# Kernel tuning notes

Measured on AMD Instinct MI355X. Metric: run time of the kernel, lower is better.

The kernel has to match this reference:

```python
import jax, jax.numpy as jnp
import numpy as np

B, N, F_IN, F_OUT = 8, 2048, 256, 128
ALPHA = 0.2  # LeakyReLU negative slope
NEG_BIG = -9e15


def setup_inputs() -> dict:
    key = jax.random.key(0)
    k1, k2, k3, k4 = jax.random.split(key, 4)
    h = jax.random.normal(k1, (B, N, F_IN), dtype=jnp.float32)
    adj = jax.random.randint(k2, (B, N, N), 0, 2, dtype=jnp.int32)
    W = jax.random.normal(k3, (F_IN, F_OUT), dtype=jnp.float32) * 0.05
    a = jax.random.normal(k4, (2 * F_OUT,), dtype=jnp.float32) * 0.05
    return {"h": h, "adj": adj, "W": W, "a": a}


def reference(h, adj, W, a):
    # Wh: [B, N, F_OUT]
    Wh = jnp.einsum("bnf,fo->bno", h, W)
    # a([Wh_i || Wh_j]) decomposes: e_ij = a1.Wh_i + a2.Wh_j  (avoids [B,N*N,2F] tensor)
    a1, a2 = a[:F_OUT], a[F_OUT:]
    s1 = jnp.einsum("bno,o->bn", Wh, a1)  # [B, N]
    s2 = jnp.einsum("bno,o->bn", Wh, a2)  # [B, N]
    e = jax.nn.leaky_relu(s1[:, :, None] + s2[:, None, :], negative_slope=ALPHA)  # [B,N,N]
    e = jnp.where(adj > 0, e, NEG_BIG)
    attention = jax.nn.softmax(e, axis=2)
    # dropout is identity (eval / p=0)
    h_prime = jnp.einsum("bij,bjo->bio", attention, Wh)  # [B, N, F_OUT]
    return h_prime
```

## Files before the change

kernel.cpp:

```cpp
#include <hip/hip_runtime.h>

#define NB 8
#define NN 2048
#define FIN 256
#define FOUT 128

typedef __attribute__((ext_vector_type(8))) short short8;
typedef __attribute__((ext_vector_type(4))) float f32x4;

static __device__ __forceinline__ unsigned short f2bf(float f) {
    unsigned int u = __float_as_uint(f);
    u += 0x7fffu + ((u >> 16) & 1u);
    return (unsigned short)(u >> 16);
}

__global__ __launch_bounds__(256) void gat_prep(
    const float* __restrict__ h, const float* __restrict__ W, const float* __restrict__ a,
    unsigned short* __restrict__ whpv, float* __restrict__ s1g, float* __restrict__ s2g)
{
    __shared__ __align__(16) float hT[64 * FIN];
    __shared__ __align__(16) unsigned short pvs[8192];
    const int t = threadIdx.x;
    const int bx = blockIdx.x;
    const int b = bx >> 5;
    const int jt = bx & 31;
    const int j0 = jt * 64;

    const float* hsrc = h + ((size_t)b * NN + j0) * FIN;
    #pragma unroll
    for (int p = 0; p < 16; ++p) {
        int idx = p * 256 + t;
        *(f32x4*)&hT[idx * 4] = *(const f32x4*)&hsrc[idx * 4];
    }
    __syncthreads();

    const int cg = t & 31;
    const int rg = t >> 5;
    float acc[8][4];
    #pragma unroll
    for (int r = 0; r < 8; ++r)
        #pragma unroll
        for (int q = 0; q < 4; ++q) acc[r][q] = 0.f;

    for (int f = 0; f < FIN; f += 4) {
        f32x4 wv[4];
        #pragma unroll
        for (int q = 0; q < 4; ++q) wv[q] = *(const f32x4*)&W[(f + q) * FOUT + cg * 4];
        #pragma unroll
        for (int r = 0; r < 8; ++r) {
            f32x4 hv = *(const f32x4*)&hT[(rg * 8 + r) * FIN + f];
            #pragma unroll
            for (int q = 0; q < 4; ++q) {
                acc[r][0] += hv[q] * wv[q][0];
                acc[r][1] += hv[q] * wv[q][1];
                acc[r][2] += hv[q] * wv[q][2];
                acc[r][3] += hv[q] * wv[q][3];
            }
        }
    }

    f32x4 a1v = *(const f32x4*)&a[cg * 4];
    f32x4 a2v = *(const f32x4*)&a[FOUT + cg * 4];
    #pragma unroll
    for (int r = 0; r < 8; ++r) {
        float p1 = acc[r][0]*a1v[0] + acc[r][1]*a1v[1] + acc[r][2]*a1v[2] + acc[r][3]*a1v[3];
        float p2 = acc[r][0]*a2v[0] + acc[r][1]*a2v[1] + acc[r][2]*a2v[2] + acc[r][3]*a2v[3];
        #pragma unroll
        for (int m = 16; m >= 1; m >>= 1) {
            p1 += __shfl_xor(p1, m, 64);
            p2 += __shfl_xor(p2, m, 64);
        }
        if (cg == 0) {
            s1g[b * NN + j0 + rg * 8 + r] = p1;
            s2g[b * NN + j0 + rg * 8 + r] = p2;
        }
    }

    #pragma unroll
    for (int r = 0; r < 8; ++r) {
        int jl = rg * 8 + r;
        int kt = jl >> 5, j5 = jl & 31, g = j5 >> 3, i = j5 & 7;
        #pragma unroll
        for (int q = 0; q < 4; ++q) {
            int c = cg * 4 + q;
            int lane = g * 16 + (c & 15);
            int nt = c >> 4;
            pvs[((kt * 8 + nt) * 64 + lane) * 8 + i] = f2bf(acc[r][q]);
        }
    }
    __syncthreads();
    unsigned short* dst = whpv + (size_t)(b * 32 + jt) * 8192;
    #pragma unroll
    for (int p = 0; p < 4; ++p) {
        int idx = p * 2048 + t * 8;
        *(short8*)&dst[idx] = *(const short8*)&pvs[idx];
    }
}

__global__ __launch_bounds__(512, 4) void gat_main(
    const int* __restrict__ adj, const unsigned short* __restrict__ whpv,
    const float* __restrict__ s1g, const float* __restrict__ s2g, float* __restrict__ out)
{
    __shared__ __align__(16) char Plds[2][32 * 128];
    __shared__ __align__(16) unsigned short BL[2][8192];
    __shared__ float Sden[32];

    const int t = threadIdx.x;
    const int bx = blockIdx.x;
    const int b = bx >> 6;
    const int i0 = (bx & 63) * 32;

    const int r  = t >> 4;
    const int jq = t & 15;

    const int lane = t & 63;
    const int w = t >> 6;
    const int mt = w & 1;
    const int nb = w >> 1;
    const int arow = mt * 16 + (lane & 15);
    const int g = lane >> 4;

    const float s1v = s1g[b * NN + i0 + r];

    f32x4 acc[2];
    acc[0] = (f32x4){0.f, 0.f, 0.f, 0.f};
    acc[1] = (f32x4){0.f, 0.f, 0.f, 0.f};
    float ssum = 0.f;

    const int* adjb = adj + (size_t)b * NN * NN + (size_t)i0 * NN;
    const int* aptr = adjb + (size_t)r * NN + jq * 4;
    const unsigned short* whb = whpv + (size_t)b * 32 * 8192;
    const float* s2b = s2g + b * NN;

    int4 ac = *(const int4*)aptr;
    short8 wc0 = *(const short8*)&whb[t * 8];
    short8 wc1 = *(const short8*)&whb[4096 + t * 8];

    const int pbyte = r * 128 + ((jq >> 1) ^ (r & 7)) * 16 + (jq & 1) * 8;
    const int abyte = arow * 128;
    int buf = 0;

    for (int jc = 0; jc < 32; ++jc) {
        const int jn = (jc + 1) & 31;
        int4 an = *(const int4*)(aptr + jn * 64);
        const unsigned short* wn = whb + (size_t)jn * 8192;
        short8 wn0 = *(const short8*)&wn[t * 8];
        short8 wn1 = *(const short8*)&wn[4096 + t * 8];

        f32x4 s2v = *(const f32x4*)&s2b[jc * 64 + jq * 4];
        float p[4];
        {
            float e0 = s1v + s2v[0]; e0 = fmaxf(e0, 0.2f * e0);
            p[0] = (ac.x > 0) ? __expf(e0) : 0.f;
            float e1 = s1v + s2v[1]; e1 = fmaxf(e1, 0.2f * e1);
            p[1] = (ac.y > 0) ? __expf(e1) : 0.f;
            float e2 = s1v + s2v[2]; e2 = fmaxf(e2, 0.2f * e2);
            p[2] = (ac.z > 0) ? __expf(e2) : 0.f;
            float e3 = s1v + s2v[3]; e3 = fmaxf(e3, 0.2f * e3);
            p[3] = (ac.w > 0) ? __expf(e3) : 0.f;
        }
        ssum += (p[0] + p[1]) + (p[2] + p[3]);
        unsigned int pk0 = (unsigned int)f2bf(p[0]) | ((unsigned int)f2bf(p[1]) << 16);
        unsigned int pk1 = (unsigned int)f2bf(p[2]) | ((unsigned int)f2bf(p[3]) << 16);
        uint2 pk = {pk0, pk1};
        *(uint2*)&Plds[buf][pbyte] = pk;

        *(short8*)&BL[buf][t * 8] = wc0;
        *(short8*)&BL[buf][4096 + t * 8] = wc1;
        __syncthreads();

        #pragma unroll
        for (int kt = 0; kt < 2; ++kt) {
            int aslot = (4 * kt + g) ^ (arow & 7);
            short8 af = *(const short8*)&Plds[buf][abyte + aslot * 16];
            #pragma unroll
            for (int n = 0; n < 2; ++n) {
                int nt = nb * 2 + n;
                short8 bfr = *(const short8*)&BL[buf][((kt * 8 + nt) * 64 + lane) * 8];
                acc[n] = __builtin_amdgcn_mfma_f32_16x16x32_bf16(af, bfr, acc[n], 0, 0, 0);
            }
        }

        ac = an; wc0 = wn0; wc1 = wn1; buf ^= 1;
    }

    {
        float v = ssum;
        #pragma unroll
        for (int m = 8; m >= 1; m >>= 1) v += __shfl_xor(v, m, 64);
        if (jq == 0) Sden[r] = v;
    }
    __syncthreads();

    float* ob = out + ((size_t)b * NN + i0) * FOUT;
    #pragma unroll
    for (int n = 0; n < 2; ++n) {
        int col = (nb * 2 + n) * 16 + (lane & 15);
        #pragma unroll
        for (int q = 0; q < 4; ++q) {
            int row = mt * 16 + (lane >> 4) * 4 + q;
            ob[(size_t)row * FOUT + col] = acc[n][q] / Sden[row];
        }
    }
}

extern "C" void kernel_launch(void* const* d_in, const int* in_sizes, int n_in,
                              void* d_out, int out_size, void* d_ws, size_t ws_size,
                              hipStream_t stream) {
    (void)in_sizes; (void)n_in; (void)out_size; (void)ws_size;
    const float* h   = (const float*)d_in[0];
    const int*   adj = (const int*)d_in[1];
    const float* W   = (const float*)d_in[2];
    const float* a   = (const float*)d_in[3];
    float* out = (float*)d_out;

    unsigned short* whpv = (unsigned short*)d_ws;
    float* s1g = (float*)((char*)d_ws + (4u << 20));
    float* s2g = (float*)((char*)d_ws + (4u << 20) + (64u << 10));

    gat_prep<<<dim3(256), dim3(256), 0, stream>>>(h, W, a, whpv, s1g, s2g);
    gat_main<<<dim3(512), dim3(512), 0, stream>>>(adj, whpv, s1g, s2g, out);
}
```

Baseline: 79.47 us.

## Batch four j-chunks per barrier with deeper prefetch and swizzled block order

```diff
diff --git a/kernel.cpp b/kernel.cpp
--- a/kernel.cpp
+++ b/kernel.cpp
@@ -13,6 +13,20 @@
     u += 0x7fffu + ((u >> 16) & 1u);
     return (unsigned short)(u >> 16);
 }
+
+static __device__ __forceinline__ unsigned int cvtpk(float lo, float hi) {
+    unsigned int d;
+    asm("v_cvt_pk_bf16_f32 %0, %1, %2" : "=v"(d) : "v"(lo), "v"(hi));
+    return d;
+}
+
+#define BAR_LGKM()                                            \
+    do {                                                      \
+        asm volatile("s_waitcnt lgkmcnt(0)" ::: "memory");    \
+        __builtin_amdgcn_sched_barrier(0);                    \
+        __builtin_amdgcn_s_barrier();                         \
+        __builtin_amdgcn_sched_barrier(0);                    \
+    } while (0)
 
 __global__ __launch_bounds__(256) void gat_prep(
     const float* __restrict__ h, const float* __restrict__ W, const float* __restrict__ a,
@@ -101,14 +115,14 @@
     const int* __restrict__ adj, const unsigned short* __restrict__ whpv,
     const float* __restrict__ s1g, const float* __restrict__ s2g, float* __restrict__ out)
 {
-    __shared__ __align__(16) char Plds[2][32 * 128];
-    __shared__ __align__(16) unsigned short BL[2][8192];
-    __shared__ float Sden[32];
+    __shared__ __align__(16) char pool[81920];
+    unsigned short* BL = (unsigned short*)pool;
+    char* Plds = pool + 65536;
 
     const int t = threadIdx.x;
     const int bx = blockIdx.x;
-    const int b = bx >> 6;
-    const int i0 = (bx & 63) * 32;
+    const int b  = bx & 7;
+    const int i0 = (bx >> 3) * 32;
 
     const int r  = t >> 4;
     const int jq = t & 15;
@@ -127,63 +141,78 @@
     acc[1] = (f32x4){0.f, 0.f, 0.f, 0.f};
     float ssum = 0.f;
 
-    const int* adjb = adj + (size_t)b * NN * NN + (size_t)i0 * NN;
-    const int* aptr = adjb + (size_t)r * NN + jq * 4;
+    const int* aptr = adj + (size_t)b * NN * NN + (size_t)(i0 + r) * NN + jq * 4;
     const unsigned short* whb = whpv + (size_t)b * 32 * 8192;
     const float* s2b = s2g + b * NN;
 
-    int4 ac = *(const int4*)aptr;
-    short8 wc0 = *(const short8*)&whb[t * 8];
-    short8 wc1 = *(const short8*)&whb[4096 + t * 8];
+    int4   ac0, ac1, ac2, ac3;
+    short8 wa0, wa1, wa2, wa3, wb0, wb1, wb2, wb3;
+    f32x4  s20, s21, s22, s23;
+
+#define PRELOAD(C)                                                          \
+    ac##C = *(const int4*)(aptr + (C) * 64);                                \
+    wa##C = *(const short8*)&whb[(size_t)(C) * 8192 + t * 8];               \
+    wb##C = *(const short8*)&whb[(size_t)(C) * 8192 + 4096 + t * 8];        \
+    s2##C = *(const f32x4*)&s2b[(C) * 64 + jq * 4];
+
+    PRELOAD(0) PRELOAD(1) PRELOAD(2) PRELOAD(3)
+#undef PRELOAD
 
     const int pbyte = r * 128 + ((jq >> 1) ^ (r & 7)) * 16 + (jq & 1) * 8;
     const int abyte = arow * 128;
-    int buf = 0;
-
-    for (int jc = 0; jc < 32; ++jc) {
-        const int jn = (jc + 1) & 31;
-        int4 an = *(const int4*)(aptr + jn * 64);
-        const unsigned short* wn = whb + (size_t)jn * 8192;
-        short8 wn0 = *(const short8*)&wn[t * 8];
-        short8 wn1 = *(const short8*)&wn[4096 + t * 8];
-
-        f32x4 s2v = *(const f32x4*)&s2b[jc * 64 + jq * 4];
-        float p[4];
-        {
-            float e0 = s1v + s2v[0]; e0 = fmaxf(e0, 0.2f * e0);
-            p[0] = (ac.x > 0) ? __expf(e0) : 0.f;
-            float e1 = s1v + s2v[1]; e1 = fmaxf(e1, 0.2f * e1);
-            p[1] = (ac.y > 0) ? __expf(e1) : 0.f;
-            float e2 = s1v + s2v[2]; e2 = fmaxf(e2, 0.2f * e2);
-            p[2] = (ac.z > 0) ? __expf(e2) : 0.f;
-            float e3 = s1v + s2v[3]; e3 = fmaxf(e3, 0.2f * e3);
-            p[3] = (ac.w > 0) ? __expf(e3) : 0.f;
-        }
-        ssum += (p[0] + p[1]) + (p[2] + p[3]);
-        unsigned int pk0 = (unsigned int)f2bf(p[0]) | ((unsigned int)f2bf(p[1]) << 16);
-        unsigned int pk1 = (unsigned int)f2bf(p[2]) | ((unsigned int)f2bf(p[3]) << 16);
-        uint2 pk = {pk0, pk1};
-        *(uint2*)&Plds[buf][pbyte] = pk;
-
-        *(short8*)&BL[buf][t * 8] = wc0;
-        *(short8*)&BL[buf][4096 + t * 8] = wc1;
-        __syncthreads();
-
-        #pragma unroll
-        for (int kt = 0; kt < 2; ++kt) {
-            int aslot = (4 * kt + g) ^ (arow & 7);
-            short8 af = *(const short8*)&Plds[buf][abyte + aslot * 16];
-            #pragma unroll
-            for (int n = 0; n < 2; ++n) {
-                int nt = nb * 2 + n;
-                short8 bfr = *(const short8*)&BL[buf][((kt * 8 + nt) * 64 + lane) * 8];
-                acc[n] = __builtin_amdgcn_mfma_f32_16x16x32_bf16(af, bfr, acc[n], 0, 0, 0);
-            }
-        }
-
-        ac = an; wc0 = wn0; wc1 = wn1; buf ^= 1;
-    }
-
+
+#define PPHASE(C, S)                                                        \
+    do {                                                                    \
+        int4   a_  = ac##C;                                                 \
+        short8 w0_ = wa##C;                                                 \
+        short8 w1_ = wb##C;                                                 \
+        f32x4  s2v = s2##C;                                                 \
+        const int jn = ((S) * 4 + 4 + (C)) & 31;                            \
+        ac##C = *(const int4*)(aptr + jn * 64);                             \
+        wa##C = *(const short8*)&whb[(size_t)jn * 8192 + t * 8];            \
+        wb##C = *(const short8*)&whb[(size_t)jn * 8192 + 4096 + t * 8];     \
+        s2##C = *(const f32x4*)&s2b[jn * 64 + jq * 4];                      \
+        float e0 = s1v + s2v[0]; e0 = fmaxf(e0, 0.2f * e0);                 \
+        float p0 = (a_.x > 0) ? __expf(e0) : 0.f;                           \
+        float e1 = s1v + s2v[1]; e1 = fmaxf(e1, 0.2f * e1);                 \
+        float p1 = (a_.y > 0) ? __expf(e1) : 0.f;                           \
+        float e2 = s1v + s2v[2]; e2 = fmaxf(e2, 0.2f * e2);                 \
+        float p2 = (a_.z > 0) ? __expf(e2) : 0.f;                           \
+        float e3 = s1v + s2v[3]; e3 = fmaxf(e3, 0.2f * e3);                 \
+        float p3 = (a_.w > 0) ? __expf(e3) : 0.f;                           \
+        ssum += (p0 + p1) + (p2 + p3);                                      \
+        uint2 pk = {cvtpk(p0, p1), cvtpk(p2, p3)};                          \
+        *(uint2*)&Plds[(C) * 4096 + pbyte] = pk;                            \
+        *(short8*)&BL[(C) * 8192 + t * 8] = w0_;                            \
+        *(short8*)&BL[(C) * 8192 + 4096 + t * 8] = w1_;                     \
+    } while (0)
+
+#define MPHASE(C)                                                           \
+    do {                                                                    \
+        _Pragma("unroll")                                                   \
+        for (int kt = 0; kt < 2; ++kt) {                                    \
+            const int aslot = (4 * kt + g) ^ (arow & 7);                    \
+            short8 af = *(const short8*)&Plds[(C) * 4096 + abyte + aslot * 16]; \
+            _Pragma("unroll")                                               \
+            for (int n = 0; n < 2; ++n) {                                   \
+                const int nt = nb * 2 + n;                                  \
+                short8 bfr = *(const short8*)&BL[(C) * 8192 + ((kt * 8 + nt) * 64 + lane) * 8]; \
+                acc[n] = __builtin_amdgcn_mfma_f32_16x16x32_bf16(af, bfr, acc[n], 0, 0, 0); \
+            }                                                               \
+        }                                                                   \
+    } while (0)
+
+    #pragma unroll 1
+    for (int s = 0; s < 8; ++s) {
+        PPHASE(0, s); PPHASE(1, s); PPHASE(2, s); PPHASE(3, s);
+        BAR_LGKM();
+        MPHASE(0); MPHASE(1); MPHASE(2); MPHASE(3);
+        BAR_LGKM();
+    }
+#undef PPHASE
+#undef MPHASE
+
+    float* Sden = (float*)pool;
     {
         float v = ssum;
         #pragma unroll
```

Measured after the change: 64.75 us. 18.5% less time.
